# Kernel optimization log

Measured on AMD Instinct MI355X. Metric: run time of the kernel, lower is better.

## Reference

```python
import jax, jax.numpy as jnp
import numpy as np

B, S, E, T, C, U, L = 2048, 50, 300, 8, 4, 300, 1000
NPAIR = E * (E - 1) // 2  # 44850
EPS = 1e-5


def setup_inputs() -> dict:
    key = jax.random.key(0)
    ks = jax.random.split(key, 18)
    r = lambda k, shape: jax.random.normal(k, shape, jnp.float32) * 0.05
    return {
        "x": jax.random.normal(ks[0], (B, S, E), jnp.float32),
        "label_embedding": jax.random.normal(ks[1], (L, U), jnp.float32),
        "fc1_w": r(ks[2], (T, E)), "fc1_b": r(ks[3], (T,)),
        "q1": jax.random.uniform(ks[4], (T,), jnp.float32),
        "fc3_w": r(ks[5], (T, E)), "fc3_b": r(ks[6], (T,)),
        "q2": jax.random.uniform(ks[7], (T,), jnp.float32),
        "fc5_w": r(ks[8], (E, 2 * E)), "fc5_b": r(ks[9], (E,)),
        "fc6_w": r(ks[10], (E, E)), "fc6_b": r(ks[11], (E,)),
        "fc7_w": r(ks[12], (E, NPAIR)), "fc7_b": r(ks[13], (E,)),
        "fc8_w": r(ks[14], (U, 2 * E)), "fc8_b": r(ks[15], (U,)),
        "v": jax.random.uniform(ks[16], (E, C), jnp.float32),
    }


def _bn(h, axes):
    # BatchNorm in training mode, fresh params (gamma=1, beta=0), biased var
    m = h.mean(axes, keepdims=True)
    var = h.var(axes, keepdims=True)
    return (h - m) * jax.lax.rsqrt(var + EPS)


def reference(x, label_embedding, fc1_w, fc1_b, q1, fc3_w, fc3_b, q2,
              fc5_w, fc5_b, fc6_w, fc6_b, fc7_w, fc7_b, fc8_w, fc8_b, v):
    pad = jnp.float32(-2 ** 32 + 1)
    sign = jnp.sign(jnp.sum(jnp.abs(x), axis=2))  # [B,S]

    def attn_pool(fw, fb, q):
        # fc -> relu -> BatchNorm1d(num_features=S) on [B,S,T] -> score -> softmax pool
        a = _bn(jax.nn.relu(jnp.einsum('bse,te->bst', x, fw) + fb), (0, 2))
        s = jnp.where(sign == 0, pad, a @ q)  # [B,S]
        w = jax.nn.softmax(s, axis=1)
        return jnp.einsum('bse,bs->be', x, w)  # [B,E]

    h = jnp.concatenate([attn_pool(fc1_w, fc1_b, q1),
                         attn_pool(fc3_w, fc3_b, q2)], axis=1)  # [B,2E]
    h5 = _bn(h @ fc5_w.T + fc5_b, (0,))       # [B,E]
    h6 = _bn(h5 @ fc6_w.T + fc6_b, (0,))      # [B,E]

    # CrossFeature: c[b,(i,j)] = h5[b,i]*h5[b,j]*(v_i . v_j), i<j row-major
    iu, ju = np.triu_indices(E, 1)
    g = jnp.sum(v[iu] * v[ju], axis=1)         # [NPAIR]
    cross = h5[:, iu] * h5[:, ju] * g          # [B,NPAIR]

    h7 = _bn(cross @ fc7_w.T + fc7_b, (0,))   # [B,E]
    out8 = jnp.concatenate([h6, h7], axis=1) @ fc8_w.T + fc8_b  # [B,U]
    return out8 @ label_embedding.T            # [B,L]
```

## Files before the change

kernel.cpp:

```cpp
#include <hip/hip_runtime.h>

#define B_ 2048
#define S_ 50
#define E_ 300
#define NPAIR 44850
#define R_ (B_ * S_)
#define PADSCORE (-4294967295.0f)
#define RSBLK 512
#define RSROWS (B_ / RSBLK)

#define NPOS 1744
#define BKSPLIT 16
#define BCPS 112

typedef _Float16 h8 __attribute__((ext_vector_type(8)));
typedef float f4 __attribute__((ext_vector_type(4)));

__device__ __forceinline__ void wf_body(
    const float* __restrict__ w, _Float16* __restrict__ Wf,
    int N, int K, int ngrp, int kt, int yblk, int t) {
  const int grp = yblk * 4 + (t >> 6);
  const int lane = t & 63, l16 = lane & 15, quad = lane >> 4;
  const int e = grp * 16 + l16;
  if (grp >= ngrp) return;
  h8 o;
  #pragma unroll
  for (int tt = 0; tt < 8; tt++) {
    int k = kt * 32 + quad * 8 + tt;
    float val = (e < N && k < K) ? w[(size_t)e * K + k] : 0.f;
    o[tt] = (_Float16)val;
  }
  *(h8*)&Wf[(((size_t)kt * ngrp + grp) * 64 + lane) * 8] = o;
}

__global__ __launch_bounds__(256) void k_prep(
    const float* __restrict__ w7, const float* __restrict__ v,
    _Float16* __restrict__ Wgf,
    const float* __restrict__ fc5w, _Float16* __restrict__ Wf5,
    const float* __restrict__ fc6w, _Float16* __restrict__ Wf6,
    const float* __restrict__ fc8w, _Float16* __restrict__ Wf8,
    const float* __restrict__ lemb, _Float16* __restrict__ WfL) {
  const int t = threadIdx.x;
  int bid = blockIdx.x;
  if (bid < NPOS * 5) {
    __shared__ float gL[32];
    const int pos = bid / 5, yblk = bid - pos * 5;
    int c = 0;
    #pragma unroll
    for (int cc = 1; cc < 10; cc++) if (pos >= 16 * cc * (cc + 1)) c = cc;
    const int i = pos - 16 * c * (c + 1), j0 = c * 32;
    if (t < 32) {
      int j = j0 + t;
      float g = 0.f;
      if (j > i && j < 300)
        g = v[i*4+0]*v[j*4+0] + v[i*4+1]*v[j*4+1] + v[i*4+2]*v[j*4+2] + v[i*4+3]*v[j*4+3];
      gL[t] = g;
    }
    __syncthreads();
    const int grp = yblk * 4 + (t >> 6);
    const int lane = t & 63, l16 = lane & 15, quad = lane >> 4;
    const int e = grp * 16 + l16;
    const int ibase = i * (599 - i) / 2 - i - 1;
    h8 outv;
    #pragma unroll
    for (int tt = 0; tt < 8; tt++) {
      int k = quad * 8 + tt;
      int j = j0 + k;
      float val = 0.f;
      if (j > i && j < 300 && e < 300)
        val = w7[(size_t)e * NPAIR + ibase + j] * gL[k];
      outv[tt] = (_Float16)val;
    }
    *(h8*)&Wgf[(((size_t)pos * 20 + grp) * 64 + lane) * 8] = outv;
    return;
  }
  bid -= NPOS * 5;
  if (bid < 95) { wf_body(fc5w, Wf5, 300, 600, 19, bid / 5, bid % 5, t); return; }
  bid -= 95;
  if (bid < 50) { wf_body(fc6w, Wf6, 300, 300, 19, bid / 5, bid % 5, t); return; }
  bid -= 50;
  if (bid < 95) { wf_body(fc8w, Wf8, 300, 600, 19, bid / 5, bid % 5, t); return; }
  bid -= 95;
  wf_body(lemb, WfL, 1000, 300, 63, bid / 16, bid % 16, t);
}

__global__ __launch_bounds__(256) void k_attn2(
    const float* __restrict__ x, const float* __restrict__ w1, const float* __restrict__ b1,
    const float* __restrict__ w3, const float* __restrict__ b3,
    float* __restrict__ a, float* __restrict__ sabs) {
  __shared__ float xs[128][68];
  __shared__ float wL[16][308];
  const int tid = threadIdx.x;
  const int r0 = blockIdx.x * 128;
  for (int u = tid; u < 16 * 75; u += 256) {
    int t = u / 75, q = u - t * 75;
    float4 v4 = (t < 8) ? *(const float4*)&w1[t * 300 + q * 4]
                        : *(const float4*)&w3[(t - 8) * 300 + q * 4];
    *(float4*)&wL[t][q * 4] = v4;
  }
  const int rg = tid >> 3, tg = tid & 7;
  float acc[4][2] = {};
  float sa[4] = {};
  for (int k0 = 0; k0 < 300; k0 += 64) {
    int w = min(64, 300 - k0);
    __syncthreads();
    #pragma unroll
    for (int it = 0; it < 8; it++) {
      int u = tid + it * 256;
      int r = u >> 4, q = u & 15;
      float4 v4 = {0.f, 0.f, 0.f, 0.f};
      if (q * 4 < w) v4 = *(const float4*)&x[(size_t)(r0 + r) * 300 + k0 + q * 4];
      *(float4*)&xs[r][q * 4] = v4;
    }
    __syncthreads();
    for (int q = 0; q < (w >> 2); q++) {
      float4 w0 = *(float4*)&wL[tg * 2][k0 + q * 4];
      float4 w1v = *(float4*)&wL[tg * 2 + 1][k0 + q * 4];
      #pragma unroll
      for (int k2 = 0; k2 < 4; k2++) {
        float4 xv = *(float4*)&xs[rg + 32 * k2][q * 4];
        acc[k2][0] += xv.x * w0.x + xv.y * w0.y + xv.z * w0.z + xv.w * w0.w;
        acc[k2][1] += xv.x * w1v.x + xv.y * w1v.y + xv.z * w1v.z + xv.w * w1v.w;
        if (tg == 0)
          sa[k2] += fabsf(xv.x) + fabsf(xv.y) + fabsf(xv.z) + fabsf(xv.w);
      }
    }
  }
  int t0 = tg * 2;
  float bb0 = (t0 < 8) ? b1[t0] : b3[t0 - 8];
  float bb1 = (t0 + 1 < 8) ? b1[t0 + 1] : b3[t0 + 1 - 8];
  #pragma unroll
  for (int k2 = 0; k2 < 4; k2++) {
    size_t r = r0 + rg + 32 * k2;
    a[r * 16 + t0]     = fmaxf(acc[k2][0] + bb0, 0.f);
    a[r * 16 + t0 + 1] = fmaxf(acc[k2][1] + bb1, 0.f);
    if (tg == 0) sabs[r] = sa[k2];
  }
}

__global__ void k_attnstats(const float* __restrict__ a, float* __restrict__ spart) {
  int s = blockIdx.x, pool = blockIdx.y, z = blockIdx.z;
  float sum = 0.f, sq = 0.f;
  for (int b = z * 512 + threadIdx.x; b < (z + 1) * 512; b += blockDim.x) {
    const float* row = &a[((size_t)b * S_ + s) * 16 + pool * 8];
    #pragma unroll
    for (int t = 0; t < 8; t++) { float v = row[t]; sum += v; sq += v * v; }
  }
  __shared__ float rs[2][4];
  int wave = threadIdx.x >> 6, lane = threadIdx.x & 63;
  #pragma unroll
  for (int off = 32; off; off >>= 1) { sum += __shfl_xor(sum, off); sq += __shfl_xor(sq, off); }
  if (lane == 0) { rs[0][wave] = sum; rs[1][wave] = sq; }
  __syncthreads();
  if (threadIdx.x == 0) {
    float S = rs[0][0] + rs[0][1] + rs[0][2] + rs[0][3];
    float Q = rs[1][0] + rs[1][1] + rs[1][2] + rs[1][3];
    spart[((size_t)(pool * S_ + s) * 4 + z) * 2 + 0] = S;
    spart[((size_t)(pool * S_ + s) * 4 + z) * 2 + 1] = Q;
  }
}

__global__ __launch_bounds__(256) void k_pool(
    const float* __restrict__ x, const float* __restrict__ a,
    const float* __restrict__ sabs, const float* __restrict__ spart,
    const float* __restrict__ q1, const float* __restrict__ q2,
    _Float16* __restrict__ hh) {
  int b = blockIdx.x;
  __shared__ float w1s[S_], w2s[S_];
  int tid = threadIdx.x;
  if (tid < S_) {
    float s1p = 0.f, q1p = 0.f, s2p = 0.f, q2p = 0.f;
    #pragma unroll
    for (int z = 0; z < 4; z++) {
      s1p += spart[((size_t)(0 * S_ + tid) * 4 + z) * 2 + 0];
      q1p += spart[((size_t)(0 * S_ + tid) * 4 + z) * 2 + 1];
      s2p += spart[((size_t)(1 * S_ + tid) * 4 + z) * 2 + 0];
      q2p += spart[((size_t)(1 * S_ + tid) * 4 + z) * 2 + 1];
    }
    const float nn = (float)(B_ * 8);
    float m1 = s1p / nn, rr1 = rsqrtf(q1p / nn - m1 * m1 + 1e-5f);
    float m2 = s2p / nn, rr2 = rsqrtf(q2p / nn - m2 * m2 + 1e-5f);
    float sc1 = 0.f, sc2 = 0.f;
    const float* r1 = &a[((size_t)b * S_ + tid) * 16];
    const float* r2 = r1 + 8;
    #pragma unroll
    for (int t = 0; t < 8; t++) {
      sc1 += (r1[t] - m1) * rr1 * q1[t];
      sc2 += (r2[t] - m2) * rr2 * q2[t];
    }
    if (sabs[(size_t)b * S_ + tid] == 0.f) { sc1 = PADSCORE; sc2 = PADSCORE; }
    w1s[tid] = sc1; w2s[tid] = sc2;
  }
  __syncthreads();
  if (tid < 64) {
    float v1 = (tid < S_) ? w1s[tid] : -3.0e38f;
    float v2 = (tid < S_) ? w2s[tid] : -3.0e38f;
    float m1 = v1, m2 = v2;
    #pragma unroll
    for (int off = 32; off; off >>= 1) {
      m1 = fmaxf(m1, __shfl_xor(m1, off));
      m2 = fmaxf(m2, __shfl_xor(m2, off));
    }
    float e1 = (tid < S_) ? expf(v1 - m1) : 0.f;
    float e2 = (tid < S_) ? expf(v2 - m2) : 0.f;
    float s1 = e1, s2 = e2;
    #pragma unroll
    for (int off = 32; off; off >>= 1) { s1 += __shfl_xor(s1, off); s2 += __shfl_xor(s2, off); }
    if (tid < S_) { w1s[tid] = e1 / s1; w2s[tid] = e2 / s2; }
  }
  __syncthreads();
  for (int e = tid; e < E_; e += 256) {
    float p1 = 0.f, p2 = 0.f;
    for (int s = 0; s < S_; s++) {
      float xv = x[((size_t)b * S_ + s) * E_ + e];
      p1 += xv * w1s[s];
      p2 += xv * w2s[s];
    }
    hh[(size_t)b * 608 + e]       = (_Float16)p1;
    hh[(size_t)b * 608 + 300 + e] = (_Float16)p2;
  }
  if (tid < 8) hh[(size_t)b * 608 + 600 + tid] = (_Float16)0.f;
}

__global__ __launch_bounds__(256) void k_gemmf(
    const _Float16* __restrict__ Xh, int ldx,
    const _Float16* __restrict__ Wf, int ngrp,
    float* __restrict__ dst, int N,
    int nchunk, int cps) {
  __shared__ _Float16 XL[64][328];
  const int mblk = blockIdx.x, nblk = blockIdx.y, ks = blockIdx.z;
  const int tid = threadIdx.x;
  const int wave = tid >> 6, lane = tid & 63, quad = lane >> 4, l16 = lane & 15;
  const int wm = wave >> 1, wn = wave & 1;
  const int ck0 = ks * cps, ck1 = min(nchunk, ck0 + cps);
  const int ncol8 = (ck1 - ck0) * 4;
  {
    const _Float16* src = Xh + (size_t)mblk * 64 * ldx + ck0 * 32;
    for (int u = tid; u < 64 * ncol8; u += 256) {
      int r = u / ncol8, c8 = u - r * ncol8;
      *(h8*)&XL[r][c8 * 8] = *(const h8*)&src[(size_t)r * ldx + c8 * 8];
    }
  }
  __syncthreads();

  f4 acc[2][5];
  #pragma unroll
  for (int i = 0; i < 2; i++)
    #pragma unroll
    for (int j = 0; j < 5; j++) acc[i][j] = (f4){0.f, 0.f, 0.f, 0.f};

  const int gbase = nblk * 10 + wn * 5;
  const _Float16* wb = Wf + ((size_t)gbase * 64 + lane) * 8;
  h8 bA[5], bB[5];
  #define LOADB(DST, CH)                                                        \
    _Pragma("unroll")                                                           \
    for (int nt = 0; nt < 5; nt++)                                              \
      DST[nt] = (gbase + nt < ngrp)                                             \
          ? *(const h8*)&wb[((size_t)(CH) * ngrp + nt) * 512]                   \
          : (h8){0, 0, 0, 0, 0, 0, 0, 0};

  if (ck0 < ck1) { LOADB(bA, ck0); }
  if (ck0 + 1 < ck1) { LOADB(bB, ck0 + 1); }

  auto step = [&](int ch, h8* bf) {
    int c0 = (ch - ck0) * 32 + quad * 8;
    h8 af[2];
    #pragma unroll
    for (int mi = 0; mi < 2; mi++)
      af[mi] = *(const h8*)&XL[wm * 32 + mi * 16 + l16][c0];
    #pragma unroll
    for (int mi = 0; mi < 2; mi++)
      #pragma unroll
      for (int nt = 0; nt < 5; nt++)
        acc[mi][nt] = __builtin_amdgcn_mfma_f32_16x16x32_f16(af[mi], bf[nt], acc[mi][nt], 0, 0, 0);
  };

  int ch = ck0;
  while (ch < ck1) {
    step(ch, bA);
    if (ch + 2 < ck1) { LOADB(bA, ch + 2); }
    ch++;
    if (ch < ck1) {
      step(ch, bB);
      if (ch + 2 < ck1) { LOADB(bB, ch + 2); }
      ch++;
    }
  }
  #undef LOADB

  float* d = dst + (size_t)ks * ((size_t)B_ * N);
  #pragma unroll
  for (int mi = 0; mi < 2; mi++) {
    int b = mblk * 64 + wm * 32 + mi * 16 + quad * 4;
    #pragma unroll
    for (int nt = 0; nt < 5; nt++) {
      int e = (gbase + nt) * 16 + l16;
      if (e < N) {
        #pragma unroll
        for (int r = 0; r < 4; r++)
          d[(size_t)(b + r) * N + e] = acc[mi][nt][r];
      }
    }
  }
}

__global__ __launch_bounds__(256) void k_reduce_stat(
    const float* __restrict__ part, float* __restrict__ pre,
    float* __restrict__ cpart, int ksp) {
  int blk = blockIdx.x;
  int r0 = blk * RSROWS;
  for (int c = threadIdx.x; c < E_; c += 256) {
    float s = 0.f, q = 0.f;
    #pragma unroll
    for (int rr = 0; rr < RSROWS; rr++) {
      int r = r0 + rr;
      float v = 0.f;
      for (int k2 = 0; k2 < ksp; k2++)
        v += part[(size_t)k2 * (B_ * E_) + (size_t)r * E_ + c];
      pre[(size_t)r * E_ + c] = v;
      s += v; q += v * v;
    }
    cpart[((size_t)blk * E_ + c) * 2 + 0] = s;
    cpart[((size_t)blk * E_ + c) * 2 + 1] = q;
  }
}

__global__ __launch_bounds__(256) void k_colstat_fin(
    const float* __restrict__ part, float* __restrict__ stat,
    int N, int nparts, int M) {
  int c = blockIdx.x;
  if (c >= N) return;
  float s = 0.f, q = 0.f;
  for (int p = threadIdx.x; p < nparts; p += 256) {
    s += part[((size_t)p * N + c) * 2 + 0];
    q += part[((size_t)p * N + c) * 2 + 1];
  }
  #pragma unroll
  for (int off = 32; off; off >>= 1) { s += __shfl_xor(s, off); q += __shfl_xor(q, off); }
  __shared__ float rs[2][4];
  int wave = threadIdx.x >> 6, lane = threadIdx.x & 63;
  if (lane == 0) { rs[0][wave] = s; rs[1][wave] = q; }
  __syncthreads();
  if (threadIdx.x == 0) {
    float S = rs[0][0] + rs[0][1] + rs[0][2] + rs[0][3];
    float Q = rs[1][0] + rs[1][1] + rs[1][2] + rs[1][3];
    float m = S / (float)M;
    float var = Q / (float)M - m * m;
    stat[c * 2 + 0] = m;
    stat[c * 2 + 1] = rsqrtf(var + 1e-5f);
  }
}

__global__ void k_norm_h5h(const float* __restrict__ X, const float* __restrict__ stat,
                           _Float16* __restrict__ h5h) {
  int idx = blockIdx.x * 256 + threadIdx.x;
  if (idx >= B_ * 320) return;
  int b = idx / 320, c = idx - b * 320;
  if (c < E_) {
    float v = (X[(size_t)b * E_ + c] - stat[c * 2]) * stat[c * 2 + 1];
    h5h[idx] = (_Float16)v;
  } else {
    h5h[idx] = (_Float16)0.f;
  }
}

__global__ void k_norm_hcat(const float* __restrict__ X, const float* __restrict__ stat,
                            _Float16* __restrict__ Y, int off, int pad) {
  int W = 300 + pad;
  int idx = blockIdx.x * 256 + threadIdx.x;
  if (idx >= B_ * W) return;
  int b = idx / W, c = idx - b * W;
  if (c < 300) {
    float v = (X[(size_t)b * E_ + c] - stat[c * 2]) * stat[c * 2 + 1];
    Y[(size_t)b * 608 + off + c] = (_Float16)v;
  } else {
    Y[(size_t)b * 608 + 600 + (c - 300)] = (_Float16)0.f;
  }
}

__global__ void k_redbias_h(const float* __restrict__ part, const float* __restrict__ bias,
                            _Float16* __restrict__ out8h, int ksp) {
  int idx = blockIdx.x * 256 + threadIdx.x;
  if (idx >= B_ * 320) return;
  int b = idx / 320, c = idx - b * 320;
  if (c < E_) {
    float s = bias[c];
    for (int k2 = 0; k2 < ksp; k2++)
      s += part[(size_t)k2 * (B_ * E_) + (size_t)b * E_ + c];
    out8h[idx] = (_Float16)s;
  } else {
    out8h[idx] = (_Float16)0.f;
  }
}

__global__ __launch_bounds__(256, 2) void k_bigmm7(
    const _Float16* __restrict__ Wgf, const _Float16* __restrict__ h5h,
    float* __restrict__ part) {
  const int n = blockIdx.x;
  const int ks = n & 15, mblk = n >> 4;
  const int tid = threadIdx.x;
  const int wave = tid >> 6, lane = tid & 63, quad = lane >> 4, l16 = lane & 15;
  const int pos0 = ks * BCPS;
  const int pos1 = min(NPOS, pos0 + BCPS);

  const int gbase = wave * 5;
  const _Float16* wb = Wgf + ((size_t)gbase * 64 + lane) * 8;

  const _Float16* rowp[4];
  #pragma unroll
  for (int mi = 0; mi < 4; mi++)
    rowp[mi] = h5h + (size_t)(mblk * 64 + mi * 16 + l16) * 320;

  f4 acc[4][5];
  #pragma unroll
  for (int i = 0; i < 4; i++)
    #pragma unroll
    for (int j = 0; j < 5; j++) acc[i][j] = (f4){0.f, 0.f, 0.f, 0.f};

  h8 bb[4][5], vjC[4], vjN[4], hi8C[4], hi8N[4];

  #define LOADB7(DST, POS)                                                     \
    _Pragma("unroll")                                                          \
    for (int nt = 0; nt < 5; nt++)                                             \
      DST[nt] = *(const h8*)&wb[(size_t)(POS) * 10240 + nt * 512];

  int c = 0, cend = 32;
  while (pos0 >= cend) { c++; cend = (c < 9) ? 16 * (c + 1) * (c + 2) : NPOS; }
  int cumc = 16 * c * (c + 1);
  #pragma unroll
  for (int mi = 0; mi < 4; mi++) {
    vjC[mi]  = *(const h8*)&rowp[mi][c * 32 + quad * 8];
    hi8C[mi] = *(const h8*)&rowp[mi][pos0 - cumc];
  }
  #pragma unroll
  for (int q = 0; q < 4; q++) { LOADB7(bb[q], pos0 + q); }

  for (int p = pos0; p < pos1; p += 8) {
    const int pn = p + 8;
    int cN = c, cendN = cend, cumcN = cumc;
    bool adv = false;
    if (pn < pos1) {
      while (pn >= cendN) {
        cN++; cendN = (cN < 9) ? 16 * (cN + 1) * (cN + 2) : NPOS; adv = true;
      }
      if (adv) cumcN = 16 * cN * (cN + 1);
      #pragma unroll
      for (int mi = 0; mi < 4; mi++)
        hi8N[mi] = *(const h8*)&rowp[mi][pn - cumcN];
      if (adv) {
        #pragma unroll
        for (int mi = 0; mi < 4; mi++)
          vjN[mi] = *(const h8*)&rowp[mi][cN * 32 + quad * 8];
      }
    }
    #pragma unroll
    for (int t = 0; t < 8; t++) {
      #pragma unroll
      for (int mi = 0; mi < 4; mi++) {
        _Float16 hsc = hi8C[mi][t];
        h8 hs = {hsc, hsc, hsc, hsc, hsc, hsc, hsc, hsc};
        h8 af = vjC[mi] * hs;
        #pragma unroll
        for (int nt = 0; nt < 5; nt++)
          acc[mi][nt] = __builtin_amdgcn_mfma_f32_16x16x32_f16(af, bb[t & 3][nt], acc[mi][nt], 0, 0, 0);
      }
      LOADB7(bb[t & 3], p + t + 4);
    }
    if (pn < pos1) {
      #pragma unroll
      for (int mi = 0; mi < 4; mi++) hi8C[mi] = hi8N[mi];
      if (adv) {
        #pragma unroll
        for (int mi = 0; mi < 4; mi++) vjC[mi] = vjN[mi];
        c = cN; cend = cendN; cumc = cumcN;
      }
    }
  }
  #undef LOADB7

  float* dst = part + (size_t)ks * (B_ * E_);
  #pragma unroll
  for (int mi = 0; mi < 4; mi++) {
    int b = mblk * 64 + mi * 16 + quad * 4;
    #pragma unroll
    for (int nt = 0; nt < 5; nt++) {
      int e = (gbase + nt) * 16 + l16;
      if (e < E_) {
        #pragma unroll
        for (int r = 0; r < 4; r++)
          dst[(size_t)(b + r) * E_ + e] = acc[mi][nt][r];
      }
    }
  }
}

extern "C" void kernel_launch(void* const* d_in, const int* in_sizes, int n_in,
                              void* d_out, int out_size, void* d_ws, size_t ws_size,
                              hipStream_t stream) {
  const float* x    = (const float*)d_in[0];
  const float* lemb = (const float*)d_in[1];
  const float* fc1w = (const float*)d_in[2];
  const float* fc1b = (const float*)d_in[3];
  const float* q1   = (const float*)d_in[4];
  const float* fc3w = (const float*)d_in[5];
  const float* fc3b = (const float*)d_in[6];
  const float* q2   = (const float*)d_in[7];
  const float* fc5w = (const float*)d_in[8];
  const float* fc6w = (const float*)d_in[10];
  const float* fc7w = (const float*)d_in[12];
  const float* fc8w = (const float*)d_in[14];
  const float* fc8b = (const float*)d_in[15];
  const float* v    = (const float*)d_in[16];
  float* out = (float*)d_out;
  (void)in_sizes; (void)n_in; (void)out_size; (void)ws_size;

  char* base = (char*)d_ws;
  size_t off = 0;
  auto alloc = [&](size_t nbytes) -> char* {
    char* p = base + off;
    off = (off + nbytes + 255) & ~(size_t)255;
    return p;
  };
  _Float16*  Wgf   = (_Float16*) alloc((size_t)(NPOS + 8) * 20 * 64 * 8 * 2);
  _Float16*  Wf5   = (_Float16*) alloc((size_t)19 * 19 * 512 * 2);
  _Float16*  Wf6   = (_Float16*) alloc((size_t)10 * 19 * 512 * 2);
  _Float16*  Wf8   = (_Float16*) alloc((size_t)19 * 19 * 512 * 2);
  _Float16*  WfL   = (_Float16*) alloc((size_t)10 * 63 * 512 * 2);
  _Float16*  hh    = (_Float16*) alloc((size_t)B_ * 608 * 2);
  _Float16*  h5h   = (_Float16*) alloc((size_t)B_ * 320 * 2);
  _Float16*  hcath = (_Float16*) alloc((size_t)B_ * 608 * 2);
  _Float16*  out8h = (_Float16*) alloc((size_t)B_ * 320 * 2);
  float*     pre   = (float*)    alloc((size_t)B_ * E_ * 4);
  float*     cpart = (float*)    alloc((size_t)RSBLK * E_ * 2 * 4);
  float*     cstat = (float*)    alloc((size_t)E_ * 2 * 4);
  size_t part_bytes = (size_t)BKSPLIT * B_ * E_ * 4;
  char* scratch = alloc(part_bytes);
  float* a     = (float*)scratch;
  float* sabs  = a + (size_t)R_ * 16;
  float* spart = sabs + R_;
  float* part  = (float*)scratch;

  hipLaunchKernelGGL(k_prep, dim3(NPOS * 5 + 95 + 50 + 95 + 160), dim3(256), 0, stream,
                     fc7w, v, Wgf, fc5w, Wf5, fc6w, Wf6, fc8w, Wf8, lemb, WfL);
  hipLaunchKernelGGL(k_attn2, dim3(R_ / 128), dim3(256), 0, stream, x, fc1w, fc1b, fc3w, fc3b, a, sabs);
  hipLaunchKernelGGL(k_attnstats, dim3(S_, 2, 4), dim3(256), 0, stream, a, spart);
  hipLaunchKernelGGL(k_pool, dim3(B_), dim3(256), 0, stream, x, a, sabs, spart, q1, q2, hh);
  hipLaunchKernelGGL(k_gemmf, dim3(32, 2, 4), dim3(256), 0, stream, hh, 608, Wf5, 19, part, 300, 19, 5);
  hipLaunchKernelGGL(k_reduce_stat, dim3(RSBLK), dim3(256), 0, stream, part, pre, cpart, 4);
  hipLaunchKernelGGL(k_colstat_fin, dim3(E_), dim3(256), 0, stream, cpart, cstat, E_, RSBLK, B_);
  hipLaunchKernelGGL(k_norm_h5h, dim3((B_ * 320) / 256), dim3(256), 0, stream, pre, cstat, h5h);
  hipLaunchKernelGGL(k_gemmf, dim3(32, 2, 4), dim3(256), 0, stream, h5h, 320, Wf6, 19, part, 300, 10, 3);
  hipLaunchKernelGGL(k_reduce_stat, dim3(RSBLK), dim3(256), 0, stream, part, pre, cpart, 4);
  hipLaunchKernelGGL(k_colstat_fin, dim3(E_), dim3(256), 0, stream, cpart, cstat, E_, RSBLK, B_);
  hipLaunchKernelGGL(k_norm_hcat, dim3((B_ * 300 + 255) / 256), dim3(256), 0, stream, pre, cstat, hcath, 0, 0);
  hipLaunchKernelGGL(k_bigmm7, dim3(BKSPLIT * 32), dim3(256), 0, stream, Wgf, h5h, part);
  hipLaunchKernelGGL(k_reduce_stat, dim3(RSBLK), dim3(256), 0, stream, part, pre, cpart, BKSPLIT);
  hipLaunchKernelGGL(k_colstat_fin, dim3(E_), dim3(256), 0, stream, cpart, cstat, E_, RSBLK, B_);
  hipLaunchKernelGGL(k_norm_hcat, dim3((B_ * 308 + 255) / 256), dim3(256), 0, stream, pre, cstat, hcath, 300, 8);
  hipLaunchKernelGGL(k_gemmf, dim3(32, 2, 4), dim3(256), 0, stream, hcath, 608, Wf8, 19, part, 300, 19, 5);
  hipLaunchKernelGGL(k_redbias_h, dim3((B_ * 320) / 256), dim3(256), 0, stream, part, fc8b, out8h, 4);
  hipLaunchKernelGGL(k_gemmf, dim3(32, 7, 1), dim3(256), 0, stream, out8h, 320, WfL, 63, out, 1000, 10, 10);
}
```

Baseline: 509.9 us.

## Replace BN statistic reduction kernels with atomics and double big-GEMM K split

Attention BN statistics are now accumulated inside k_attn2 through shared-memory atomics followed by global atomics, which removes the separate k_attnstats kernel. The column statistics for fc5, fc6 and fc7 are accumulated with global atomics in k_reduce_stat, and the normalization kernels compute mean and rsqrt inline, which removes three k_colstat_fin launches. The big cross-feature GEMM now splits K 32 ways instead of 16 and requests 4 blocks per SM for more parallelism. In exchange the split-K partial buffer and its reduction traffic double, and atomic contention plus non-deterministic float summation order are introduced.

```diff
diff --git a/kernel.cpp b/kernel.cpp
--- a/kernel.cpp
+++ b/kernel.cpp
@@ -10,8 +10,8 @@
 #define RSROWS (B_ / RSBLK)
 
 #define NPOS 1744
-#define BKSPLIT 16
-#define BCPS 112
+#define BKSPLIT 32
+#define BCPS 56
 
 typedef _Float16 h8 __attribute__((ext_vector_type(8)));
 typedef float f4 __attribute__((ext_vector_type(4)));
@@ -39,9 +39,15 @@
     const float* __restrict__ fc5w, _Float16* __restrict__ Wf5,
     const float* __restrict__ fc6w, _Float16* __restrict__ Wf6,
     const float* __restrict__ fc8w, _Float16* __restrict__ Wf8,
-    const float* __restrict__ lemb, _Float16* __restrict__ WfL) {
+    const float* __restrict__ lemb, _Float16* __restrict__ WfL,
+    float* __restrict__ spart, float* __restrict__ cs5,
+    float* __restrict__ cs6, float* __restrict__ cs7) {
   const int t = threadIdx.x;
   int bid = blockIdx.x;
+  if (bid == 0) { for (int u = t; u < 200; u += 256) spart[u] = 0.f; }
+  else if (bid == 1) { for (int u = t; u < 600; u += 256) cs5[u] = 0.f; }
+  else if (bid == 2) { for (int u = t; u < 600; u += 256) cs6[u] = 0.f; }
+  else if (bid == 3) { for (int u = t; u < 600; u += 256) cs7[u] = 0.f; }
   if (bid < NPOS * 5) {
     __shared__ float gL[32];
     const int pos = bid / 5, yblk = bid - pos * 5;
@@ -87,9 +93,10 @@
 __global__ __launch_bounds__(256) void k_attn2(
     const float* __restrict__ x, const float* __restrict__ w1, const float* __restrict__ b1,
     const float* __restrict__ w3, const float* __restrict__ b3,
-    float* __restrict__ a, float* __restrict__ sabs) {
+    float* __restrict__ a, float* __restrict__ sabs, float* __restrict__ spart) {
   __shared__ float xs[128][68];
   __shared__ float wL[16][308];
+  __shared__ float sst[200];
   const int tid = threadIdx.x;
   const int r0 = blockIdx.x * 128;
   for (int u = tid; u < 16 * 75; u += 256) {
@@ -98,6 +105,7 @@
                         : *(const float4*)&w3[(t - 8) * 300 + q * 4];
     *(float4*)&wL[t][q * 4] = v4;
   }
+  for (int u = tid; u < 200; u += 256) sst[u] = 0.f;
   const int rg = tid >> 3, tg = tid & 7;
   float acc[4][2] = {};
   float sa[4] = {};
@@ -129,35 +137,22 @@
   int t0 = tg * 2;
   float bb0 = (t0 < 8) ? b1[t0] : b3[t0 - 8];
   float bb1 = (t0 + 1 < 8) ? b1[t0 + 1] : b3[t0 + 1 - 8];
+  const int pool = tg >> 2;
   #pragma unroll
   for (int k2 = 0; k2 < 4; k2++) {
     size_t r = r0 + rg + 32 * k2;
-    a[r * 16 + t0]     = fmaxf(acc[k2][0] + bb0, 0.f);
-    a[r * 16 + t0 + 1] = fmaxf(acc[k2][1] + bb1, 0.f);
+    float v0 = fmaxf(acc[k2][0] + bb0, 0.f);
+    float v1 = fmaxf(acc[k2][1] + bb1, 0.f);
+    a[r * 16 + t0]     = v0;
+    a[r * 16 + t0 + 1] = v1;
     if (tg == 0) sabs[r] = sa[k2];
-  }
-}
-
-__global__ void k_attnstats(const float* __restrict__ a, float* __restrict__ spart) {
-  int s = blockIdx.x, pool = blockIdx.y, z = blockIdx.z;
-  float sum = 0.f, sq = 0.f;
-  for (int b = z * 512 + threadIdx.x; b < (z + 1) * 512; b += blockDim.x) {
-    const float* row = &a[((size_t)b * S_ + s) * 16 + pool * 8];
-    #pragma unroll
-    for (int t = 0; t < 8; t++) { float v = row[t]; sum += v; sq += v * v; }
-  }
-  __shared__ float rs[2][4];
-  int wave = threadIdx.x >> 6, lane = threadIdx.x & 63;
-  #pragma unroll
-  for (int off = 32; off; off >>= 1) { sum += __shfl_xor(sum, off); sq += __shfl_xor(sq, off); }
-  if (lane == 0) { rs[0][wave] = sum; rs[1][wave] = sq; }
+    int s = (int)(r % 50);
+    atomicAdd(&sst[(pool * S_ + s) * 2 + 0], v0 + v1);
+    atomicAdd(&sst[(pool * S_ + s) * 2 + 1], v0 * v0 + v1 * v1);
+  }
   __syncthreads();
-  if (threadIdx.x == 0) {
-    float S = rs[0][0] + rs[0][1] + rs[0][2] + rs[0][3];
-    float Q = rs[1][0] + rs[1][1] + rs[1][2] + rs[1][3];
-    spart[((size_t)(pool * S_ + s) * 4 + z) * 2 + 0] = S;
-    spart[((size_t)(pool * S_ + s) * 4 + z) * 2 + 1] = Q;
-  }
+  for (int u = tid; u < 200; u += 256)
+    atomicAdd(&spart[u], sst[u]);
 }
 
 __global__ __launch_bounds__(256) void k_pool(
@@ -169,17 +164,11 @@
   __shared__ float w1s[S_], w2s[S_];
   int tid = threadIdx.x;
   if (tid < S_) {
-    float s1p = 0.f, q1p = 0.f, s2p = 0.f, q2p = 0.f;
-    #pragma unroll
-    for (int z = 0; z < 4; z++) {
-      s1p += spart[((size_t)(0 * S_ + tid) * 4 + z) * 2 + 0];
-      q1p += spart[((size_t)(0 * S_ + tid) * 4 + z) * 2 + 1];
-      s2p += spart[((size_t)(1 * S_ + tid) * 4 + z) * 2 + 0];
-      q2p += spart[((size_t)(1 * S_ + tid) * 4 + z) * 2 + 1];
-    }
     const float nn = (float)(B_ * 8);
-    float m1 = s1p / nn, rr1 = rsqrtf(q1p / nn - m1 * m1 + 1e-5f);
-    float m2 = s2p / nn, rr2 = rsqrtf(q2p / nn - m2 * m2 + 1e-5f);
+    float S1 = spart[(0 * S_ + tid) * 2 + 0], Q1 = spart[(0 * S_ + tid) * 2 + 1];
+    float S2 = spart[(1 * S_ + tid) * 2 + 0], Q2 = spart[(1 * S_ + tid) * 2 + 1];
+    float m1 = S1 / nn, rr1 = rsqrtf(Q1 / nn - m1 * m1 + 1e-5f);
+    float m2 = S2 / nn, rr2 = rsqrtf(Q2 / nn - m2 * m2 + 1e-5f);
     float sc1 = 0.f, sc2 = 0.f;
     const float* r1 = &a[((size_t)b * S_ + tid) * 16];
     const float* r2 = r1 + 8;
@@ -306,7 +295,7 @@
 
 __global__ __launch_bounds__(256) void k_reduce_stat(
     const float* __restrict__ part, float* __restrict__ pre,
-    float* __restrict__ cpart, int ksp) {
+    float* __restrict__ cs, int ksp) {
   int blk = blockIdx.x;
   int r0 = blk * RSROWS;
   for (int c = threadIdx.x; c < E_; c += 256) {
@@ -320,59 +309,39 @@
       pre[(size_t)r * E_ + c] = v;
       s += v; q += v * v;
     }
-    cpart[((size_t)blk * E_ + c) * 2 + 0] = s;
-    cpart[((size_t)blk * E_ + c) * 2 + 1] = q;
-  }
-}
-
-__global__ __launch_bounds__(256) void k_colstat_fin(
-    const float* __restrict__ part, float* __restrict__ stat,
-    int N, int nparts, int M) {
-  int c = blockIdx.x;
-  if (c >= N) return;
-  float s = 0.f, q = 0.f;
-  for (int p = threadIdx.x; p < nparts; p += 256) {
-    s += part[((size_t)p * N + c) * 2 + 0];
-    q += part[((size_t)p * N + c) * 2 + 1];
-  }
-  #pragma unroll
-  for (int off = 32; off; off >>= 1) { s += __shfl_xor(s, off); q += __shfl_xor(q, off); }
-  __shared__ float rs[2][4];
-  int wave = threadIdx.x >> 6, lane = threadIdx.x & 63;
-  if (lane == 0) { rs[0][wave] = s; rs[1][wave] = q; }
-  __syncthreads();
-  if (threadIdx.x == 0) {
-    float S = rs[0][0] + rs[0][1] + rs[0][2] + rs[0][3];
-    float Q = rs[1][0] + rs[1][1] + rs[1][2] + rs[1][3];
-    float m = S / (float)M;
-    float var = Q / (float)M - m * m;
-    stat[c * 2 + 0] = m;
-    stat[c * 2 + 1] = rsqrtf(var + 1e-5f);
-  }
-}
-
-__global__ void k_norm_h5h(const float* __restrict__ X, const float* __restrict__ stat,
+    atomicAdd(&cs[c * 2 + 0], s);
+    atomicAdd(&cs[c * 2 + 1], q);
+  }
+}
+
+__global__ void k_norm_h5h(const float* __restrict__ X, const float* __restrict__ cs,
                            _Float16* __restrict__ h5h) {
   int idx = blockIdx.x * 256 + threadIdx.x;
   if (idx >= B_ * 320) return;
   int b = idx / 320, c = idx - b * 320;
   if (c < E_) {
-    float v = (X[(size_t)b * E_ + c] - stat[c * 2]) * stat[c * 2 + 1];
-    h5h[idx] = (_Float16)v;
+    float S = cs[c * 2], Q = cs[c * 2 + 1];
+    float m = S / (float)B_;
+    float rr = rsqrtf(Q / (float)B_ - m * m + 1e-5f);
+    h5h[idx] = (_Float16)((X[(size_t)b * E_ + c] - m) * rr);
   } else {
     h5h[idx] = (_Float16)0.f;
   }
 }
 
-__global__ void k_norm_hcat(const float* __restrict__ X, const float* __restrict__ stat,
-                            _Float16* __restrict__ Y, int off, int pad) {
+__global__ void k_norm_hcat(float* __restrict__ X, const float* __restrict__ cs,
+                            _Float16* __restrict__ Y, int off, int pad, int zeroX) {
   int W = 300 + pad;
   int idx = blockIdx.x * 256 + threadIdx.x;
   if (idx >= B_ * W) return;
   int b = idx / W, c = idx - b * W;
   if (c < 300) {
-    float v = (X[(size_t)b * E_ + c] - stat[c * 2]) * stat[c * 2 + 1];
-    Y[(size_t)b * 608 + off + c] = (_Float16)v;
+    float S = cs[c * 2], Q = cs[c * 2 + 1];
+    float m = S / (float)B_;
+    float rr = rsqrtf(Q / (float)B_ - m * m + 1e-5f);
+    float v = X[(size_t)b * E_ + c];
+    Y[(size_t)b * 608 + off + c] = (_Float16)((v - m) * rr);
+    if (zeroX) X[(size_t)b * E_ + c] = 0.f;
   } else {
     Y[(size_t)b * 608 + 600 + (c - 300)] = (_Float16)0.f;
   }
@@ -393,11 +362,11 @@
   }
 }
 
-__global__ __launch_bounds__(256, 2) void k_bigmm7(
+__global__ __launch_bounds__(256, 4) void k_bigmm8(
     const _Float16* __restrict__ Wgf, const _Float16* __restrict__ h5h,
     float* __restrict__ part) {
   const int n = blockIdx.x;
-  const int ks = n & 15, mblk = n >> 4;
+  const int ks = n & 31, mblk = n >> 5;
   const int tid = threadIdx.x;
   const int wave = tid >> 6, lane = tid & 63, quad = lane >> 4, l16 = lane & 15;
   const int pos0 = ks * BCPS;
@@ -419,7 +388,7 @@
 
   h8 bb[4][5], vjC[4], vjN[4], hi8C[4], hi8N[4];
 
-  #define LOADB7(DST, POS)                                                     \
+  #define LOADB8(DST, POS)                                                     \
     _Pragma("unroll")                                                          \
     for (int nt = 0; nt < 5; nt++)                                             \
       DST[nt] = *(const h8*)&wb[(size_t)(POS) * 10240 + nt * 512];
@@ -433,7 +402,7 @@
     hi8C[mi] = *(const h8*)&rowp[mi][pos0 - cumc];
   }
   #pragma unroll
-  for (int q = 0; q < 4; q++) { LOADB7(bb[q], pos0 + q); }
+  for (int q = 0; q < 4; q++) { LOADB8(bb[q], pos0 + q); }
 
   for (int p = pos0; p < pos1; p += 8) {
     const int pn = p + 8;
@@ -464,7 +433,7 @@
         for (int nt = 0; nt < 5; nt++)
           acc[mi][nt] = __builtin_amdgcn_mfma_f32_16x16x32_f16(af, bb[t & 3][nt], acc[mi][nt], 0, 0, 0);
       }
-      LOADB7(bb[t & 3], p + t + 4);
+      LOADB8(bb[t & 3], p + t + 4);
     }
     if (pn < pos1) {
       #pragma unroll
@@ -476,7 +445,7 @@
       }
     }
   }
-  #undef LOADB7
+  #undef LOADB8
 
   float* dst = part + (size_t)ks * (B_ * E_);
   #pragma unroll
@@ -531,8 +500,9 @@
   _Float16*  hcath = (_Float16*) alloc((size_t)B_ * 608 * 2);
   _Float16*  out8h = (_Float16*) alloc((size_t)B_ * 320 * 2);
   float*     pre   = (float*)    alloc((size_t)B_ * E_ * 4);
-  float*     cpart = (float*)    alloc((size_t)RSBLK * E_ * 2 * 4);
-  float*     cstat = (float*)    alloc((size_t)E_ * 2 * 4);
+  float*     cs5   = (float*)    alloc((size_t)600 * 4);
+  float*     cs6   = (float*)    alloc((size_t)600 * 4);
+  float*     cs7   = (float*)    alloc((size_t)600 * 4);
   size_t part_bytes = (size_t)BKSPLIT * B_ * E_ * 4;
   char* scratch = alloc(part_bytes);
   float* a     = (float*)scratch;
@@ -541,22 +511,19 @@
   float* part  = (float*)scratch;
 
   hipLaunchKernelGGL(k_prep, dim3(NPOS * 5 + 95 + 50 + 95 + 160), dim3(256), 0, stream,
-                     fc7w, v, Wgf, fc5w, Wf5, fc6w, Wf6, fc8w, Wf8, lemb, WfL);
-  hipLaunchKernelGGL(k_attn2, dim3(R_ / 128), dim3(256), 0, stream, x, fc1w, fc1b, fc3w, fc3b, a, sabs);
-  hipLaunchKernelGGL(k_attnstats, dim3(S_, 2, 4), dim3(256), 0, stream, a, spart);
+                     fc7w, v, Wgf, fc5w, Wf5, fc6w, Wf6, fc8w, Wf8, lemb, WfL,
+                     spart, cs5, cs6, cs7);
+  hipLaunchKernelGGL(k_attn2, dim3(R_ / 128), dim3(256), 0, stream, x, fc1w, fc1b, fc3w, fc3b, a, sabs, spart);
   hipLaunchKernelGGL(k_pool, dim3(B_), dim3(256), 0, stream, x, a, sabs, spart, q1, q2, hh);
   hipLaunchKernelGGL(k_gemmf, dim3(32, 2, 4), dim3(256), 0, stream, hh, 608, Wf5, 19, part, 300, 19, 5);
-  hipLaunchKernelGGL(k_reduce_stat, dim3(RSBLK), dim3(256), 0, stream, part, pre, cpart, 4);
-  hipLaunchKernelGGL(k_colstat_fin, dim3(E_), dim3(256), 0, stream, cpart, cstat, E_, RSBLK, B_);
-  hipLaunchKernelGGL(k_norm_h5h, dim3((B_ * 320) / 256), dim3(256), 0, stream, pre, cstat, h5h);
+  hipLaunchKernelGGL(k_reduce_stat, dim3(RSBLK), dim3(256), 0, stream, part, pre, cs5, 4);
+  hipLaunchKernelGGL(k_norm_h5h, dim3((B_ * 320) / 256), dim3(256), 0, stream, pre, cs5, h5h);
   hipLaunchKernelGGL(k_gemmf, dim3(32, 2, 4), dim3(256), 0, stream, h5h, 320, Wf6, 19, part, 300, 10, 3);
-  hipLaunchKernelGGL(k_reduce_stat, dim3(RSBLK), dim3(256), 0, stream, part, pre, cpart, 4);
-  hipLaunchKernelGGL(k_colstat_fin, dim3(E_), dim3(256), 0, stream, cpart, cstat, E_, RSBLK, B_);
-  hipLaunchKernelGGL(k_norm_hcat, dim3((B_ * 300 + 255) / 256), dim3(256), 0, stream, pre, cstat, hcath, 0, 0);
-  hipLaunchKernelGGL(k_bigmm7, dim3(BKSPLIT * 32), dim3(256), 0, stream, Wgf, h5h, part);
-  hipLaunchKernelGGL(k_reduce_stat, dim3(RSBLK), dim3(256), 0, stream, part, pre, cpart, BKSPLIT);
-  hipLaunchKernelGGL(k_colstat_fin, dim3(E_), dim3(256), 0, stream, cpart, cstat, E_, RSBLK, B_);
-  hipLaunchKernelGGL(k_norm_hcat, dim3((B_ * 308 + 255) / 256), dim3(256), 0, stream, pre, cstat, hcath, 300, 8);
+  hipLaunchKernelGGL(k_reduce_stat, dim3(RSBLK), dim3(256), 0, stream, part, pre, cs6, 4);
+  hipLaunchKernelGGL(k_norm_hcat, dim3((B_ * 300 + 255) / 256), dim3(256), 0, stream, pre, cs6, hcath, 0, 0, 0);
+  hipLaunchKernelGGL(k_bigmm8, dim3(BKSPLIT * 32), dim3(256), 0, stream, Wgf, h5h, part);
+  hipLaunchKernelGGL(k_reduce_stat, dim3(RSBLK), dim3(256), 0, stream, part, pre, cs7, BKSPLIT);
+  hipLaunchKernelGGL(k_norm_hcat, dim3((B_ * 308 + 255) / 256), dim3(256), 0, stream, pre, cs7, hcath, 300, 8, 0);
   hipLaunchKernelGGL(k_gemmf, dim3(32, 2, 4), dim3(256), 0, stream, hcath, 608, Wf8, 19, part, 300, 19, 5);
   hipLaunchKernelGGL(k_redbias_h, dim3((B_ * 320) / 256), dim3(256), 0, stream, part, fc8b, out8h, 4);
   hipLaunchKernelGGL(k_gemmf, dim3(32, 7, 1), dim3(256), 0, stream, out8h, 320, WfL, 63, out, 1000, 10, 10);
```

After: 1.467 ms. 2.88x slower.
